# Performance work log

Hardware: AMD Instinct MI355X
Metric: run time of the kernel (lower is better)

The kernel has to match this reference:

```python
import jax, jax.numpy as jnp
import numpy as np

N_NODES = 100000
N_EDGES = 1600000
IN_CH = 48
OUT_CH = 64
K = 2


def setup_inputs() -> dict:
    key = jax.random.key(0)
    k1, k2, k3, k4 = jax.random.split(key, 4)
    x = jax.random.normal(k1, (N_NODES, IN_CH), dtype=jnp.float32)
    edge_index = jax.random.randint(k2, (2, N_EDGES), 0, N_NODES, dtype=jnp.int64)
    W = jax.random.normal(k3, (IN_CH, OUT_CH), dtype=jnp.float32) * (1.0 / np.sqrt(IN_CH))
    b = jax.random.normal(k4, (OUT_CH,), dtype=jnp.float32) * 0.01
    return {"x": x, "edge_index": edge_index, "W": W, "b": b}


def _propagate(x, row, col):
    n = x.shape[0]
    # degree of each node counted over col (destination) indices
    deg = jax.ops.segment_sum(jnp.ones_like(col, dtype=x.dtype), col, num_segments=n)
    deg_inv_sqrt = jnp.where(deg > 0, jax.lax.rsqrt(jnp.where(deg > 0, deg, 1.0)), 0.0)
    norm = deg_inv_sqrt[row] * deg_inv_sqrt[col]  # [E]
    # gather-scale-scatter: out[col] += x[row] * norm
    msgs = x[row] * norm[:, None]  # [E, d]
    return jax.ops.segment_sum(msgs, col, num_segments=n)


def reference(x, edge_index, W, b):
    row, col = edge_index[0], edge_index[1]
    h = x
    for _ in range(K):
        h = _propagate(h, row, col)
    return h @ W + b
```

## Files before the change

kernel.cpp:

```cpp
#include <hip/hip_runtime.h>
#include <hip/hip_bf16.h>
#include <hip/hip_fp16.h>


#define N_NODES 100000
#define N_EDGES 1600000
#define IN_CH 48
#define OUT_CH 64
#define NBUCKETS 392
#define CAP 4608
#define EPB 2048
#define EPR 8
#define NBLK_EDGE 782
#define NBLK_BKT 391
#define RSTRIDE 32

__global__ void init_kernel(int* __restrict__ bucketCursor, int* __restrict__ binTotal) {
    int t = threadIdx.x;
    if (t < NBUCKETS) bucketCursor[t] = t * CAP;
    if (t < 64) binTotal[t] = 0;
}

__global__ void bucket_scatter_kernel(const int* __restrict__ row, const int* __restrict__ col,
                                      int* __restrict__ bucketCursor, int* __restrict__ edge_packed) {
    __shared__ int lh[NBUCKETS];
    __shared__ int lofs[NBUCKETS];
    __shared__ int lbase[NBUCKETS];
    __shared__ int stage[EPB];
    __shared__ unsigned short sbkt[EPB];
    __shared__ int wsum[4];
    int tid = threadIdx.x;
    int base = blockIdx.x * EPB;
    for (int i = tid; i < NBUCKETS; i += 256) lh[i] = 0;
    __syncthreads();
    #pragma unroll
    for (int k = 0; k < EPR; k++) {
        int e = base + k * 256 + tid;
        if (e < N_EDGES) atomicAdd(&lh[col[e] >> 8], 1);
    }
    __syncthreads();
    {
        int c0 = (tid < 196) ? lh[2 * tid] : 0;
        int c1 = (tid < 196) ? lh[2 * tid + 1] : 0;
        int s = c0 + c1;
        int incl = s;
        int lane = tid & 63, w = tid >> 6;
        #pragma unroll
        for (int o = 1; o < 64; o <<= 1) {
            int v = __shfl_up(incl, o, 64);
            if (lane >= o) incl += v;
        }
        if (lane == 63) wsum[w] = incl;
        __syncthreads();
        int wbase = 0;
        for (int k = 0; k < w; k++) wbase += wsum[k];
        int ex = wbase + incl - s;
        if (tid < 196) {
            lofs[2 * tid]     = ex;
            lofs[2 * tid + 1] = ex + c0;
        }
    }
    __syncthreads();
    for (int i = tid; i < NBUCKETS; i += 256) {
        int c = lh[i];
        if (c > 0) lbase[i] = atomicAdd(&bucketCursor[i], c);
        lh[i] = 0;
    }
    __syncthreads();
    #pragma unroll
    for (int k = 0; k < EPR; k++) {
        int e = base + k * 256 + tid;
        if (e < N_EDGES) {
            int c = col[e];
            int bkt = c >> 8;
            int r = atomicAdd(&lh[bkt], 1);
            int slot = lofs[bkt] + r;
            stage[slot] = (row[e] << 8) | (c & 255);
            sbkt[slot] = (unsigned short)bkt;
        }
    }
    __syncthreads();
    int total = (base + EPB <= N_EDGES) ? EPB : (N_EDGES - base);
    for (int i = tid; i < total; i += 256) {
        int bkt = sbkt[i];
        int dst = lbase[bkt] + (i - lofs[bkt]);
        if (dst < (bkt + 1) * CAP)
            edge_packed[dst] = stage[i];
    }
}

__global__ void fine_sort_kernel(const int* __restrict__ edge_packed,
                                 const int* __restrict__ bucketCursor,
                                 int* __restrict__ edge_src,
                                 int* __restrict__ deg, int* __restrict__ start,
                                 float* __restrict__ dis, int* __restrict__ binTotal) {
    __shared__ int fh[256];
    __shared__ int cur[256];
    __shared__ int bh[64];
    __shared__ int wsum2[4];
    int b = blockIdx.x;
    int t = threadIdx.x;
    int s0 = b * CAP;
    int s1 = min(bucketCursor[b], (b + 1) * CAP);
    int nodeBase = b << 8;
    fh[t] = 0;
    if (t < 64) bh[t] = 0;
    __syncthreads();
    for (int j = s0 + t; j < s1; j += 256)
        atomicAdd(&fh[edge_packed[j] & 255], 1);
    __syncthreads();
    int c = fh[t];
    int incl = c;
    {
        int sl = t & 63, sw = t >> 6;
        #pragma unroll
        for (int o = 1; o < 64; o <<= 1) {
            int v = __shfl_up(incl, o, 64);
            if (sl >= o) incl += v;
        }
        if (sl == 63) wsum2[sw] = incl;
        __syncthreads();
        int wbase = 0;
        for (int k = 0; k < sw; k++) wbase += wsum2[k];
        incl += wbase;
    }
    int ex = incl - c;
    int node = nodeBase + t;
    bool valid = (node < N_NODES);
    int d = c;
    float dv = (valid && d > 0) ? rsqrtf((float)d) : 0.0f;
    cur[t] = ex;
    if (valid) {
        deg[node] = d;
        start[node] = s0 + ex;
        dis[node] = dv;
        atomicAdd(&bh[min(d, 63)], 1);
    }
    __syncthreads();
    for (int j = s0 + t; j < s1; j += 256) {
        int rc = edge_packed[j];
        int p = atomicAdd(&cur[rc & 255], 1);
        edge_src[s0 + p] = rc >> 8;
    }
    __syncthreads();
    if (t < 64 && bh[t]) atomicAdd(&binTotal[t], bh[t]);
}

__global__ void scale_kernel(const float* __restrict__ x, const float* __restrict__ dis,
                             __half2* __restrict__ xs) {
    int g = blockIdx.x * 32 + (threadIdx.x >> 3);
    int c = (threadIdx.x & 7) * 3;
    float dd = dis[g];
    const float2* px = (const float2*)x + g * 24 + c;
    float2 v0 = px[0], v1 = px[1], v2 = px[2];
    __half2* q = xs + g * RSTRIDE + c;
    q[0] = __floats2half2_rn(v0.x * dd, v0.y * dd);
    q[1] = __floats2half2_rn(v1.x * dd, v1.y * dd);
    q[2] = __floats2half2_rn(v2.x * dd, v2.y * dd);
}

__global__ void binscan_kernel(const int* __restrict__ binTotal, int* __restrict__ binCursor) {
    if (threadIdx.x == 0) {
        int s = 0;
        for (int k = 63; k >= 0; k--) { binCursor[k] = s; s += binTotal[k]; }
    }
}

__global__ void order_kernel(const int* __restrict__ deg, const int* __restrict__ start,
                             const float* __restrict__ dis, int* __restrict__ binCursor,
                             int4* __restrict__ nodeinfo, int n) {
    __shared__ int lhist[64];
    __shared__ int lbase[64];
    int i = blockIdx.x * 256 + threadIdx.x;
    if (threadIdx.x < 64) lhist[threadIdx.x] = 0;
    __syncthreads();
    int bin = 0, myrank = 0;
    if (i < n) {
        bin = min(deg[i], 63);
        myrank = atomicAdd(&lhist[bin], 1);
    }
    __syncthreads();
    if (threadIdx.x < 64 && lhist[threadIdx.x] > 0)
        lbase[threadIdx.x] = atomicAdd(&binCursor[threadIdx.x], lhist[threadIdx.x]);
    __syncthreads();
    if (i < n)
        nodeinfo[lbase[bin] + myrank] = make_int4(i, start[i], deg[i], __float_as_int(dis[i]));
}

#define LOAD3(p, v0, v1, v2) { v0 = (p)[0]; v1 = (p)[1]; v2 = (p)[2]; }
#define ACC6(v0, v1, v2) { \
    float2 u0 = __half22float2(v0), u1 = __half22float2(v1), u2 = __half22float2(v2); \
    a0 += u0.x; a1 += u0.y; a2 += u1.x; a3 += u1.y; a4 += u2.x; a5 += u2.y; }
#define ACC6B(v0, v1, v2) { \
    float2 u0 = __half22float2(v0), u1 = __half22float2(v1), u2 = __half22float2(v2); \
    b0 += u0.x; b1 += u0.y; b2 += u1.x; b3 += u1.y; b4 += u2.x; b5 += u2.y; }

#define DECLD(P) __half2 P##00,P##01,P##02,P##10,P##11,P##12,P##20,P##21,P##22,P##30,P##31,P##32
#define DECLS(S) int S##0, S##1, S##2, S##3
#define LOADSRC(S) { S##0 = edge_src[j]; S##1 = edge_src[j+1]; \
                     S##2 = edge_src[j+2]; S##3 = edge_src[j+3]; j += 4; }
#define ISSUED(P, S, basep) { \
    const __half2* q0 = basep + S##0 * RSTRIDE + lane3; \
    const __half2* q1 = basep + S##1 * RSTRIDE + lane3; \
    const __half2* q2 = basep + S##2 * RSTRIDE + lane3; \
    const __half2* q3 = basep + S##3 * RSTRIDE + lane3; \
    P##00 = q0[0]; P##01 = q0[1]; P##02 = q0[2]; \
    P##10 = q1[0]; P##11 = q1[1]; P##12 = q1[2]; \
    P##20 = q2[0]; P##21 = q2[1]; P##22 = q2[2]; \
    P##30 = q3[0]; P##31 = q3[1]; P##32 = q3[2]; }
#define CONSUMED(P) { ACC6(P##00,P##01,P##02); ACC6B(P##10,P##11,P##12); \
                      ACC6(P##20,P##21,P##22); ACC6B(P##30,P##31,P##32); }

#define GATHER_PIPELINE(basep) { \
    int m = (e - s) >> 2; \
    DECLD(A); DECLD(B); \
    DECLS(sa); DECLS(sb); \
    if (m >= 2) { \
        LOADSRC(sa); LOADSRC(sb); \
        ISSUED(A, sa, basep); \
        m -= 2; \
        while (m >= 2) { \
            LOADSRC(sa); \
            ISSUED(B, sb, basep); \
            CONSUMED(A); \
            LOADSRC(sb); \
            ISSUED(A, sa, basep); \
            CONSUMED(B); \
            m -= 2; \
        } \
        if (m == 1) { \
            LOADSRC(sa); \
            ISSUED(B, sb, basep); \
            CONSUMED(A); \
            ISSUED(A, sa, basep); \
            CONSUMED(B); \
            CONSUMED(A); \
        } else { \
            ISSUED(B, sb, basep); \
            CONSUMED(A); \
            CONSUMED(B); \
        } \
    } else if (m == 1) { \
        LOADSRC(sa); \
        ISSUED(A, sa, basep); \
        CONSUMED(A); \
    } \
    for (; j < e; ++j) { \
        const __half2* p0 = basep + edge_src[j] * RSTRIDE + lane3; \
        __half2 v00, v01, v02; \
        LOAD3(p0, v00, v01, v02); \
        ACC6(v00, v01, v02); \
    } \
    a0 += b0; a1 += b1; a2 += b2; a3 += b3; a4 += b4; a5 += b5; }

__global__ void gather1_kernel(const __half2* __restrict__ xs,
                               const int* __restrict__ edge_src,
                               const int4* __restrict__ nodeinfo,
                               __half2* __restrict__ h1) {
    int g = blockIdx.x * 32 + (threadIdx.x >> 3);
    int lane3 = (threadIdx.x & 7) * 3;
    int4 ni = nodeinfo[g];
    int node = ni.x, s = ni.y, e = s + ni.z;
    float dv = __int_as_float(ni.w);
    float a0 = 0, a1 = 0, a2 = 0, a3 = 0, a4 = 0, a5 = 0;
    float b0 = 0, b1 = 0, b2 = 0, b3 = 0, b4 = 0, b5 = 0;
    int j = s;
    GATHER_PIPELINE(xs);
    float sc = dv * dv;
    __half2* q = h1 + node * RSTRIDE + lane3;
    q[0] = __floats2half2_rn(a0 * sc, a1 * sc);
    q[1] = __floats2half2_rn(a2 * sc, a3 * sc);
    q[2] = __floats2half2_rn(a4 * sc, a5 * sc);
}

__global__ void gather2_gemm_kernel(const __half2* __restrict__ h1,
                                    const int* __restrict__ edge_src,
                                    const int4* __restrict__ nodeinfo,
                                    const float* __restrict__ W,
                                    const float* __restrict__ bias,
                                    float* __restrict__ out) {
    __shared__ float sW[IN_CH * OUT_CH];
    __shared__ float sb[OUT_CH];
    __shared__ float sh[32][IN_CH + 1];

    for (int i = threadIdx.x; i < IN_CH * OUT_CH; i += 256) sW[i] = W[i];
    if (threadIdx.x < OUT_CH) sb[threadIdx.x] = bias[threadIdx.x];

    int nl = threadIdx.x >> 3;
    int lane = threadIdx.x & 7;
    int lane3 = lane * 3;
    int g = blockIdx.x * 32 + nl;
    int4 ni = nodeinfo[g];
    int node = ni.x, s = ni.y, e = s + ni.z;
    float dv = __int_as_float(ni.w);

    float a0 = 0, a1 = 0, a2 = 0, a3 = 0, a4 = 0, a5 = 0;
    float b0 = 0, b1 = 0, b2 = 0, b3 = 0, b4 = 0, b5 = 0;
    int j = s;
    GATHER_PIPELINE(h1);
    int c0 = 6 * lane;
    sh[nl][c0 + 0] = a0 * dv;
    sh[nl][c0 + 1] = a1 * dv;
    sh[nl][c0 + 2] = a2 * dv;
    sh[nl][c0 + 3] = a3 * dv;
    sh[nl][c0 + 4] = a4 * dv;
    sh[nl][c0 + 5] = a5 * dv;
    __syncthreads();

    int j0 = lane * 8;
    float acc[8];
    #pragma unroll
    for (int i = 0; i < 8; i++) acc[i] = sb[j0 + i];
    for (int k = 0; k < IN_CH; k++) {
        float s0 = sh[nl][k];
        #pragma unroll
        for (int i = 0; i < 8; i++) acc[i] += s0 * sW[k * OUT_CH + j0 + i];
    }
    float4* o = (float4*)(out + (size_t)node * OUT_CH + j0);
    o[0] = make_float4(acc[0], acc[1], acc[2], acc[3]);
    o[1] = make_float4(acc[4], acc[5], acc[6], acc[7]);
}

extern "C" void kernel_launch(void* const* d_in, const int* in_sizes, int n_in,
                              void* d_out, int out_size, void* d_ws, size_t ws_size,
                              hipStream_t stream) {
    const float* x   = (const float*)d_in[0];
    const int*   ei  = (const int*)d_in[1];
    const float* W   = (const float*)d_in[2];
    const float* b   = (const float*)d_in[3];
    float* out = (float*)d_out;

    const int* row = ei;
    const int* col = ei + N_EDGES;

    int* ws_i = (int*)d_ws;
    int* bucketCursor = ws_i;
    int* binTotal     = ws_i + 512;
    int* binCursor    = ws_i + 576;
    int* deg          = ws_i + 1024;
    int* start        = ws_i + 101376;
    float* dis        = (float*)(ws_i + 201728);
    int4* nodeinfo    = (int4*)(ws_i + 302080);
    int* edge_packed  = ws_i + 703488;
    __half2* xs       = (__half2*)(ws_i + 703488);
    int* edge_src     = ws_i + 3903488;
    __half2* h1       = (__half2*)(ws_i + 5709824);

    init_kernel<<<1, 512, 0, stream>>>(bucketCursor, binTotal);
    bucket_scatter_kernel<<<NBLK_EDGE, 256, 0, stream>>>(row, col, bucketCursor, edge_packed);
    fine_sort_kernel<<<NBLK_BKT, 256, 0, stream>>>(edge_packed, bucketCursor,
                                                   edge_src, deg, start, dis, binTotal);
    scale_kernel<<<N_NODES / 32, 256, 0, stream>>>(x, dis, xs);
    binscan_kernel<<<1, 64, 0, stream>>>(binTotal, binCursor);
    order_kernel<<<(N_NODES + 255) / 256, 256, 0, stream>>>(deg, start, dis, binCursor,
                                                            nodeinfo, N_NODES);

    gather1_kernel<<<N_NODES / 32, 256, 0, stream>>>(xs, edge_src, nodeinfo, h1);
    gather2_gemm_kernel<<<N_NODES / 32, 256, 0, stream>>>(h1, edge_src, nodeinfo, W, b, out);
}
```

Before: 211.2 us.

## Replace two-level bucket sort with global atomic histogram, scan, and atomic permutation

Replaces the bucketed coarse/fine counting sort with a CSR build: a global atomic degree histogram, a two-level prefix scan for start offsets, and a permutation kernel that places each edge via a global atomicAdd on a per-node cursor. This removes the shared-memory staging and the bucket capacity limit, at the cost of 3.2M global atomics and scattered writes. Edge order within a node becomes nondeterministic, and writes to edge_src lose the locality the bucket staging gave.

Result: slower. 366.2 us (+73.4%).

```diff
diff --git a/kernel.cpp b/kernel.cpp
--- a/kernel.cpp
+++ b/kernel.cpp
@@ -7,143 +7,117 @@
 #define N_EDGES 1600000
 #define IN_CH 48
 #define OUT_CH 64
-#define NBUCKETS 392
-#define CAP 4608
-#define EPB 2048
-#define EPR 8
-#define NBLK_EDGE 782
-#define NBLK_BKT 391
+#define NNP 100352
+#define NBLK_SCAN 392
+#define NBLK_EDGE 6250
 #define RSTRIDE 32
 
-__global__ void init_kernel(int* __restrict__ bucketCursor, int* __restrict__ binTotal) {
+__global__ void zero_kernel(int* __restrict__ deg, int* __restrict__ binTotal) {
+    int i = blockIdx.x * 256 + threadIdx.x;
+    if (i < NNP) deg[i] = 0;
+    if (i < 64) binTotal[i] = 0;
+}
+
+__global__ void hist_kernel(const int* __restrict__ col, int* __restrict__ deg) {
+    int i = blockIdx.x * 256 + threadIdx.x;
+    atomicAdd(&deg[col[i]], 1);
+}
+
+__global__ void scanA_kernel(const int* __restrict__ deg, int* __restrict__ start,
+                             int* __restrict__ blockSum) {
+    __shared__ int wsum[4];
+    int b = blockIdx.x, t = threadIdx.x;
+    int i = b * 256 + t;
+    int c = deg[i];
+    int incl = c;
+    int sl = t & 63, sw = t >> 6;
+    #pragma unroll
+    for (int o = 1; o < 64; o <<= 1) {
+        int v = __shfl_up(incl, o, 64);
+        if (sl >= o) incl += v;
+    }
+    if (sl == 63) wsum[sw] = incl;
+    __syncthreads();
+    int wbase = 0;
+    for (int k = 0; k < sw; k++) wbase += wsum[k];
+    incl += wbase;
+    start[i] = incl - c;
+    if (t == 255) blockSum[b] = incl;
+}
+
+__global__ void scanB_kernel(int* __restrict__ blockSum) {
+    __shared__ int wsum[8];
     int t = threadIdx.x;
-    if (t < NBUCKETS) bucketCursor[t] = t * CAP;
-    if (t < 64) binTotal[t] = 0;
-}
-
-__global__ void bucket_scatter_kernel(const int* __restrict__ row, const int* __restrict__ col,
-                                      int* __restrict__ bucketCursor, int* __restrict__ edge_packed) {
-    __shared__ int lh[NBUCKETS];
-    __shared__ int lofs[NBUCKETS];
-    __shared__ int lbase[NBUCKETS];
-    __shared__ int stage[EPB];
-    __shared__ unsigned short sbkt[EPB];
-    __shared__ int wsum[4];
-    int tid = threadIdx.x;
-    int base = blockIdx.x * EPB;
-    for (int i = tid; i < NBUCKETS; i += 256) lh[i] = 0;
-    __syncthreads();
+    int c = (t < NBLK_SCAN) ? blockSum[t] : 0;
+    int incl = c;
+    int sl = t & 63, sw = t >> 6;
     #pragma unroll
-    for (int k = 0; k < EPR; k++) {
-        int e = base + k * 256 + tid;
-        if (e < N_EDGES) atomicAdd(&lh[col[e] >> 8], 1);
-    }
-    __syncthreads();
-    {
-        int c0 = (tid < 196) ? lh[2 * tid] : 0;
-        int c1 = (tid < 196) ? lh[2 * tid + 1] : 0;
-        int s = c0 + c1;
-        int incl = s;
-        int lane = tid & 63, w = tid >> 6;
-        #pragma unroll
-        for (int o = 1; o < 64; o <<= 1) {
-            int v = __shfl_up(incl, o, 64);
-            if (lane >= o) incl += v;
-        }
-        if (lane == 63) wsum[w] = incl;
-        __syncthreads();
-        int wbase = 0;
-        for (int k = 0; k < w; k++) wbase += wsum[k];
-        int ex = wbase + incl - s;
-        if (tid < 196) {
-            lofs[2 * tid]     = ex;
-            lofs[2 * tid + 1] = ex + c0;
-        }
-    }
-    __syncthreads();
-    for (int i = tid; i < NBUCKETS; i += 256) {
-        int c = lh[i];
-        if (c > 0) lbase[i] = atomicAdd(&bucketCursor[i], c);
-        lh[i] = 0;
-    }
-    __syncthreads();
-    #pragma unroll
-    for (int k = 0; k < EPR; k++) {
-        int e = base + k * 256 + tid;
-        if (e < N_EDGES) {
-            int c = col[e];
-            int bkt = c >> 8;
-            int r = atomicAdd(&lh[bkt], 1);
-            int slot = lofs[bkt] + r;
-            stage[slot] = (row[e] << 8) | (c & 255);
-            sbkt[slot] = (unsigned short)bkt;
-        }
-    }
-    __syncthreads();
-    int total = (base + EPB <= N_EDGES) ? EPB : (N_EDGES - base);
-    for (int i = tid; i < total; i += 256) {
-        int bkt = sbkt[i];
-        int dst = lbase[bkt] + (i - lofs[bkt]);
-        if (dst < (bkt + 1) * CAP)
-            edge_packed[dst] = stage[i];
-    }
-}
-
-__global__ void fine_sort_kernel(const int* __restrict__ edge_packed,
-                                 const int* __restrict__ bucketCursor,
-                                 int* __restrict__ edge_src,
-                                 int* __restrict__ deg, int* __restrict__ start,
-                                 float* __restrict__ dis, int* __restrict__ binTotal) {
-    __shared__ int fh[256];
-    __shared__ int cur[256];
+    for (int o = 1; o < 64; o <<= 1) {
+        int v = __shfl_up(incl, o, 64);
+        if (sl >= o) incl += v;
+    }
+    if (sl == 63) wsum[sw] = incl;
+    __syncthreads();
+    int wbase = 0;
+    for (int k = 0; k < sw; k++) wbase += wsum[k];
+    incl += wbase;
+    if (t < NBLK_SCAN) blockSum[t] = incl - c;
+}
+
+__global__ void cur_kernel(const int* __restrict__ deg, const int* __restrict__ blockSum,
+                           int* __restrict__ start, int* __restrict__ cur,
+                           float* __restrict__ dis, int* __restrict__ binTotal) {
     __shared__ int bh[64];
-    __shared__ int wsum2[4];
-    int b = blockIdx.x;
-    int t = threadIdx.x;
-    int s0 = b * CAP;
-    int s1 = min(bucketCursor[b], (b + 1) * CAP);
-    int nodeBase = b << 8;
-    fh[t] = 0;
+    int b = blockIdx.x, t = threadIdx.x;
     if (t < 64) bh[t] = 0;
     __syncthreads();
-    for (int j = s0 + t; j < s1; j += 256)
-        atomicAdd(&fh[edge_packed[j] & 255], 1);
-    __syncthreads();
-    int c = fh[t];
-    int incl = c;
-    {
-        int sl = t & 63, sw = t >> 6;
-        #pragma unroll
-        for (int o = 1; o < 64; o <<= 1) {
-            int v = __shfl_up(incl, o, 64);
-            if (sl >= o) incl += v;
-        }
-        if (sl == 63) wsum2[sw] = incl;
-        __syncthreads();
-        int wbase = 0;
-        for (int k = 0; k < sw; k++) wbase += wsum2[k];
-        incl += wbase;
-    }
-    int ex = incl - c;
-    int node = nodeBase + t;
-    bool valid = (node < N_NODES);
-    int d = c;
-    float dv = (valid && d > 0) ? rsqrtf((float)d) : 0.0f;
-    cur[t] = ex;
-    if (valid) {
-        deg[node] = d;
-        start[node] = s0 + ex;
-        dis[node] = dv;
-        atomicAdd(&bh[min(d, 63)], 1);
-    }
-    __syncthreads();
-    for (int j = s0 + t; j < s1; j += 256) {
-        int rc = edge_packed[j];
-        int p = atomicAdd(&cur[rc & 255], 1);
-        edge_src[s0 + p] = rc >> 8;
-    }
+    int i = b * 256 + t;
+    int s = start[i] + blockSum[b];
+    start[i] = s;
+    cur[i] = s;
+    int d = deg[i];
+    bool valid = (i < N_NODES);
+    dis[i] = (valid && d > 0) ? rsqrtf((float)d) : 0.0f;
+    if (valid) atomicAdd(&bh[min(d, 63)], 1);
     __syncthreads();
     if (t < 64 && bh[t]) atomicAdd(&binTotal[t], bh[t]);
+}
+
+__global__ void binscan_kernel(const int* __restrict__ binTotal, int* __restrict__ binCursor) {
+    if (threadIdx.x == 0) {
+        int s = 0;
+        for (int k = 63; k >= 0; k--) { binCursor[k] = s; s += binTotal[k]; }
+    }
+}
+
+__global__ void order_kernel(const int* __restrict__ deg, const int* __restrict__ start,
+                             const float* __restrict__ dis, int* __restrict__ binCursor,
+                             int4* __restrict__ nodeinfo, int n) {
+    __shared__ int lhist[64];
+    __shared__ int lbase[64];
+    int i = blockIdx.x * 256 + threadIdx.x;
+    if (threadIdx.x < 64) lhist[threadIdx.x] = 0;
+    __syncthreads();
+    int bin = 0, myrank = 0;
+    if (i < n) {
+        bin = min(deg[i], 63);
+        myrank = atomicAdd(&lhist[bin], 1);
+    }
+    __syncthreads();
+    if (threadIdx.x < 64 && lhist[threadIdx.x] > 0)
+        lbase[threadIdx.x] = atomicAdd(&binCursor[threadIdx.x], lhist[threadIdx.x]);
+    __syncthreads();
+    if (i < n)
+        nodeinfo[lbase[bin] + myrank] = make_int4(i, start[i], deg[i], __float_as_int(dis[i]));
+}
+
+__global__ void perm_kernel(const int* __restrict__ row, const int* __restrict__ col,
+                            int* __restrict__ cur, int* __restrict__ edge_src) {
+    int i = blockIdx.x * 256 + threadIdx.x;
+    int c = col[i];
+    int r = row[i];
+    int p = atomicAdd(&cur[c], 1);
+    edge_src[p] = r;
 }
 
 __global__ void scale_kernel(const float* __restrict__ x, const float* __restrict__ dis,
@@ -157,34 +131,6 @@
     q[0] = __floats2half2_rn(v0.x * dd, v0.y * dd);
     q[1] = __floats2half2_rn(v1.x * dd, v1.y * dd);
     q[2] = __floats2half2_rn(v2.x * dd, v2.y * dd);
-}
-
-__global__ void binscan_kernel(const int* __restrict__ binTotal, int* __restrict__ binCursor) {
-    if (threadIdx.x == 0) {
-        int s = 0;
-        for (int k = 63; k >= 0; k--) { binCursor[k] = s; s += binTotal[k]; }
-    }
-}
-
-__global__ void order_kernel(const int* __restrict__ deg, const int* __restrict__ start,
-                             const float* __restrict__ dis, int* __restrict__ binCursor,
-                             int4* __restrict__ nodeinfo, int n) {
-    __shared__ int lhist[64];
-    __shared__ int lbase[64];
-    int i = blockIdx.x * 256 + threadIdx.x;
-    if (threadIdx.x < 64) lhist[threadIdx.x] = 0;
-    __syncthreads();
-    int bin = 0, myrank = 0;
-    if (i < n) {
-        bin = min(deg[i], 63);
-        myrank = atomicAdd(&lhist[bin], 1);
-    }
-    __syncthreads();
-    if (threadIdx.x < 64 && lhist[threadIdx.x] > 0)
-        lbase[threadIdx.x] = atomicAdd(&binCursor[threadIdx.x], lhist[threadIdx.x]);
-    __syncthreads();
-    if (i < n)
-        nodeinfo[lbase[bin] + myrank] = make_int4(i, start[i], deg[i], __float_as_int(dis[i]));
 }
 
 #define LOAD3(p, v0, v1, v2) { v0 = (p)[0]; v1 = (p)[1]; v2 = (p)[2]; }
@@ -334,26 +280,28 @@
     const int* col = ei + N_EDGES;
 
     int* ws_i = (int*)d_ws;
-    int* bucketCursor = ws_i;
-    int* binTotal     = ws_i + 512;
-    int* binCursor    = ws_i + 576;
-    int* deg          = ws_i + 1024;
-    int* start        = ws_i + 101376;
-    float* dis        = (float*)(ws_i + 201728);
-    int4* nodeinfo    = (int4*)(ws_i + 302080);
-    int* edge_packed  = ws_i + 703488;
-    __half2* xs       = (__half2*)(ws_i + 703488);
-    int* edge_src     = ws_i + 3903488;
-    __half2* h1       = (__half2*)(ws_i + 5709824);
-
-    init_kernel<<<1, 512, 0, stream>>>(bucketCursor, binTotal);
-    bucket_scatter_kernel<<<NBLK_EDGE, 256, 0, stream>>>(row, col, bucketCursor, edge_packed);
-    fine_sort_kernel<<<NBLK_BKT, 256, 0, stream>>>(edge_packed, bucketCursor,
-                                                   edge_src, deg, start, dis, binTotal);
-    scale_kernel<<<N_NODES / 32, 256, 0, stream>>>(x, dis, xs);
+    int* deg          = ws_i;
+    int* start        = ws_i + 100352;
+    int* cur          = ws_i + 200704;
+    float* dis        = (float*)(ws_i + 301056);
+    int* blockSum     = ws_i + 401408;
+    int* binTotal     = ws_i + 401920;
+    int* binCursor    = ws_i + 401984;
+    int4* nodeinfo    = (int4*)(ws_i + 402048);
+    int* edge_src     = ws_i + 803456;
+    __half2* xs       = (__half2*)(ws_i + 2403456);
+    __half2* h1       = (__half2*)(ws_i + 5603456);
+
+    zero_kernel<<<NBLK_SCAN, 256, 0, stream>>>(deg, binTotal);
+    hist_kernel<<<NBLK_EDGE, 256, 0, stream>>>(col, deg);
+    scanA_kernel<<<NBLK_SCAN, 256, 0, stream>>>(deg, start, blockSum);
+    scanB_kernel<<<1, 512, 0, stream>>>(blockSum);
+    cur_kernel<<<NBLK_SCAN, 256, 0, stream>>>(deg, blockSum, start, cur, dis, binTotal);
     binscan_kernel<<<1, 64, 0, stream>>>(binTotal, binCursor);
     order_kernel<<<(N_NODES + 255) / 256, 256, 0, stream>>>(deg, start, dis, binCursor,
                                                             nodeinfo, N_NODES);
+    perm_kernel<<<NBLK_EDGE, 256, 0, stream>>>(row, col, cur, edge_src);
+    scale_kernel<<<N_NODES / 32, 256, 0, stream>>>(x, dis, xs);
 
     gather1_kernel<<<N_NODES / 32, 256, 0, stream>>>(xs, edge_src, nodeinfo, h1);
     gather2_gemm_kernel<<<N_NODES / 32, 256, 0, stream>>>(h1, edge_src, nodeinfo, W, b, out);
```
